# Kernel tuning notes

Hardware: AMD Instinct MI355X
Metric: run time of the kernel (lower is better)

Reference implementation:

```python
import jax, jax.numpy as jnp
import numpy as np

B, U = 2048, 4096
BUDGET_POS = 24.0
BUDGET_NEG = 24.0


def setup_inputs() -> dict:
    key = jax.random.key(0)
    k1, k2, k3 = jax.random.split(key, 3)
    unit_duration_exec = jax.random.uniform(k1, (B, U), dtype=jnp.float32) * 10.0
    source_duration_obs = jax.random.randint(k2, (B, U), 0, 20, dtype=jnp.int32)
    unit_mask = jnp.ones((B, U), dtype=jnp.float32)
    speech_commit_mask = jax.random.randint(k3, (B, U), 0, 2, dtype=jnp.int32)
    residual_prev = jnp.zeros((B, 1), dtype=jnp.float32)
    prefix_offset_prev = jnp.zeros((B, 1), dtype=jnp.float32)
    return {
        'unit_duration_exec': unit_duration_exec,
        'source_duration_obs': source_duration_obs,
        'unit_mask': unit_mask,
        'speech_commit_mask': speech_commit_mask,
        'residual_prev': residual_prev,
        'prefix_offset_prev': prefix_offset_prev,
    }


def _project_row(dur, src, cm, scm, carry0, off0):
    # Sequential per-unit duration clamp/carry scan for a single batch row.
    def step(carry, xs):
        c, off = carry
        d, s, m, sm = xs
        src_count = jnp.maximum(0.0, jnp.round(s))          # int(max(0, round(src)))
        total = jnp.maximum(0.0, d + c)
        frames0 = jnp.maximum(1.0, jnp.floor(total))
        anchor = jnp.maximum(1.0, src_count)
        lower = jnp.maximum(1.0, jnp.ceil(anchor - (BUDGET_NEG + off)))
        upper = jnp.maximum(lower, jnp.floor(anchor + (BUDGET_POS - off)))
        frames = jnp.clip(frames0, lower, upper)
        is_commit = m > 0.5
        is_speech = sm > 0.5
        active = is_commit & is_speech                        # committed speech unit
        proj = jnp.where(is_commit, jnp.where(is_speech, frames, src_count), 0.0)
        c_next = jnp.where(active, total - frames, c)
        off_next = jnp.where(active, off + frames - anchor, off)
        return (c_next, off_next), proj

    (c_f, off_f), proj = jax.lax.scan(step, (carry0, off0), (dur, src, cm, sm_f := scm))
    return proj, c_f, off_f


def reference(unit_duration_exec, source_duration_obs, unit_mask, speech_commit_mask,
              residual_prev, prefix_offset_prev):
    commit_mask = unit_mask  # sealed_mask is None -> commit_mask = unit_mask.float()
    src = source_duration_obs.astype(jnp.float32)
    scm = speech_commit_mask.astype(jnp.float32)
    carry0 = residual_prev[:, 0]
    off0 = jnp.round(prefix_offset_prev[:, 0])  # int(round(prev offset))

    projected, residual_next, offset_next = jax.vmap(_project_row)(
        unit_duration_exec, src, commit_mask, scm, carry0, off0)

    # materialized = x + stop_grad(projected*mask - x)  (straight-through)
    projected_prefix = projected * commit_mask
    materialized = unit_duration_exec + jax.lax.stop_gradient(
        projected_prefix - unit_duration_exec)
    cached_duration_exec = projected * commit_mask
    return (materialized, projected, cached_duration_exec,
            residual_next[:, None], offset_next[:, None])
```

## Files before the change

### kernel.cpp

```cpp
#include <hip/hip_runtime.h>
#include <stdint.h>


__device__ __forceinline__ float rl_f(float v, int lane) {
  return __int_as_float(__builtin_amdgcn_readlane(__float_as_int(v), lane));
}

__global__ __launch_bounds__(64, 2)
void sdp_scan_kernel(const float* __restrict__ dur, const int* __restrict__ src,
                     const float* __restrict__ um, const int* __restrict__ scm,
                     const float* __restrict__ res_prev,
                     const float* __restrict__ off_prev,
                     float* __restrict__ out, int B, int U) {
  const int row  = blockIdx.x;
  const int lane = threadIdx.x;

  const int tot = B * U;
  float* __restrict__ outM = out;
  float* __restrict__ outP = out + tot;
  float* __restrict__ outC = out + 2 * tot;

  float c = res_prev[row];
  float w = rintf(off_prev[row]) + 24.0f;

  const int rowbase = row * U;
  const int rowlast = rowbase + U - 1;
  const int ntiles  = (U + 63) >> 6;

  int u    = lane;
  int idx  = rowbase + lane;
  int idxc = idx <= rowlast ? idx : rowlast;
  float d = dur[idxc]; int s = src[idxc]; float m = um[idxc]; int q = scm[idxc];

  for (int tile = 0; tile < ntiles; ++tile) {
    const int nidx  = idx + 64;
    const int nidxc = nidx <= rowlast ? nidx : rowlast;
    float dn = dur[nidxc]; int sn = src[nidxc];
    float mn = um[nidxc];  int qn = scm[nidxc];
    __builtin_amdgcn_sched_barrier(0);

    const bool valid = u < U;
    const float srcc   = fmaxf(0.0f, (float)s);
    const float anchor = fmaxf(1.0f, srcc);
    const bool  ic     = m > 0.5f;
    const bool  act    = valid && ic && (q > 0);

    const unsigned long long bal = __ballot(act);
    const int n = __popcll(bal);
    const int below = __builtin_amdgcn_mbcnt_hi((unsigned)(bal >> 32),
                      __builtin_amdgcn_mbcnt_lo((unsigned)bal, 0));
    const int pidx = (act ? below : n + (lane - below)) << 2;
    const float vdc = __int_as_float(__builtin_amdgcn_ds_permute(pidx, __float_as_int(d)));
    const float vac = __int_as_float(__builtin_amdgcn_ds_permute(pidx, __float_as_int(anchor)));

    const float vprev = __int_as_float(
        __builtin_amdgcn_ds_bpermute(((lane - 1) & 63) << 2, __float_as_int(vac)));
    const unsigned long long condm = __ballot(vdc <= vprev);

    float projc = vac;
    int j = 0;
    while (j < n) {
      const float dj = rl_f(vdc, j);
      if (w == 0.0f && c + dj <= 0.0f) {
        const unsigned long long above =
            (j >= 63) ? 0ull : ((~condm) >> (j + 1));
        int mEnd = above ? (j + 1 + (int)__builtin_ctzll(above)) : 64;
        if (mEnd > n) mEnd = n;
        c = 0.0f - rl_f(vac, mEnd - 1);
        j = mEnd;
      } else {
        const float at = rl_f(vac, j);
        const float lo = at - w;
        const float up = lo + 48.0f;
        const float total  = fmaxf(0.0f, c + dj);
        const float f0     = fmaxf(1.0f, floorf(total));
        const float frames = fminf(fmaxf(f0, lo), up);
        c = total - frames;
        w = frames - lo;
        projc = (lane == j) ? frames : projc;
        ++j;
      }
    }

    const float pf = __int_as_float(
        __builtin_amdgcn_ds_bpermute(below << 2, __float_as_int(projc)));
    const float proj = act ? pf : (ic ? srcc : 0.0f);

    if (valid) {
      const float pm = proj * m;
      const float mt = d + (pm - d);
      outM[idx] = mt;
      outP[idx] = proj;
      outC[idx] = pm;
    }

    d = dn; s = sn; m = mn; q = qn;
    idx = nidx; u += 64;
  }

  if (lane == 0) {
    out[3 * tot + row]     = c;
    out[3 * tot + B + row] = w - 24.0f;
  }
}

extern "C" void kernel_launch(void* const* d_in, const int* in_sizes, int n_in,
                              void* d_out, int out_size, void* d_ws, size_t ws_size,
                              hipStream_t stream) {
  const float* dur      = (const float*)d_in[0];
  const int*   src      = (const int*)d_in[1];
  const float* um       = (const float*)d_in[2];
  const int*   scm      = (const int*)d_in[3];
  const float* res_prev = (const float*)d_in[4];
  const float* off_prev = (const float*)d_in[5];
  float* out = (float*)d_out;

  const int B = in_sizes[4];
  const int U = in_sizes[0] / B;

  dim3 grid(B);
  dim3 block(64);
  sdp_scan_kernel<<<grid, block, 0, stream>>>(dur, src, um, scm, res_prev, off_prev,
                                              out, B, U);
}
```

Measured before the change: 300.3 us.

## Split each row scan into speculative segments with a repair pass

Each row's sequential scan is split into 8 segments that run in parallel. Every segment starts from a guessed carry state taken from the last active unit of the previous tile, and it records its exit state after each tile. A second kernel walks the segments per row, checks whether the guessed entry state matches the true carry, and recomputes only the mismatched tiles until the state reconverges with the recorded one. This adds parallelism across the long serial row, at the cost of extra workspace traffic, a second launch, and possible rework when the speculation is wrong. The tile-level software prefetch of the old loop is dropped.

Result: faster. 249.3 us (-17.0%).

```diff
diff --git a/kernel.cpp b/kernel.cpp
--- a/kernel.cpp
+++ b/kernel.cpp
@@ -2,17 +2,89 @@
 #include <stdint.h>
 
 
+#define NSEG 8
+
 __device__ __forceinline__ float rl_f(float v, int lane) {
   return __int_as_float(__builtin_amdgcn_readlane(__float_as_int(v), lane));
 }
 
-__global__ __launch_bounds__(64, 2)
-void sdp_scan_kernel(const float* __restrict__ dur, const int* __restrict__ src,
+__device__ __forceinline__ void proc_tile(
+    const float* __restrict__ dur, const int* __restrict__ src,
+    const float* __restrict__ um, const int* __restrict__ scm,
+    float* __restrict__ outM, float* __restrict__ outP, float* __restrict__ outC,
+    int tilebase, int rowlast, int lane, float& c, float& w) {
+  const int  idx   = tilebase + lane;
+  const bool valid = idx <= rowlast;
+  const int  idxc  = valid ? idx : rowlast;
+  const float d = dur[idxc];
+  const int   s = src[idxc];
+  const float m = um[idxc];
+  const int   q = scm[idxc];
+
+  const float srcc   = fmaxf(0.0f, (float)s);
+  const float anchor = fmaxf(1.0f, srcc);
+  const bool  ic     = m > 0.5f;
+  const bool  act    = valid && ic && (q > 0);
+
+  const unsigned long long bal = __ballot(act);
+  const int n = __popcll(bal);
+  const int below = __builtin_amdgcn_mbcnt_hi((unsigned)(bal >> 32),
+                    __builtin_amdgcn_mbcnt_lo((unsigned)bal, 0));
+  const int pidx = (act ? below : n + (lane - below)) << 2;
+  const float vdc = __int_as_float(__builtin_amdgcn_ds_permute(pidx, __float_as_int(d)));
+  const float vac = __int_as_float(__builtin_amdgcn_ds_permute(pidx, __float_as_int(anchor)));
+  const float vprev = __int_as_float(
+      __builtin_amdgcn_ds_bpermute(((lane - 1) & 63) << 2, __float_as_int(vac)));
+  const unsigned long long condm = __ballot(vdc <= vprev);
+
+  float projc = vac;
+  int j = 0;
+  while (j < n) {
+    const float dj = rl_f(vdc, j);
+    if (w == 0.0f && c + dj <= 0.0f) {
+      const unsigned long long above = (j >= 63) ? 0ull : ((~condm) >> (j + 1));
+      int mEnd = above ? (j + 1 + (int)__builtin_ctzll(above)) : 64;
+      if (mEnd > n) mEnd = n;
+      c = 0.0f - rl_f(vac, mEnd - 1);
+      j = mEnd;
+    } else {
+      const float at = rl_f(vac, j);
+      const float lo = at - w;
+      const float up = lo + 48.0f;
+      const float total  = fmaxf(0.0f, c + dj);
+      const float f0     = fmaxf(1.0f, floorf(total));
+      const float frames = fminf(fmaxf(f0, lo), up);
+      c = total - frames;
+      w = frames - lo;
+      projc = (lane == j) ? frames : projc;
+      ++j;
+    }
+  }
+
+  const float pf = __int_as_float(
+      __builtin_amdgcn_ds_bpermute(below << 2, __float_as_int(projc)));
+  const float proj = act ? pf : (ic ? srcc : 0.0f);
+  if (valid) {
+    const float pm = __fmul_rn(proj, m);
+    const float mt = __fadd_rn(d, __fsub_rn(pm, d));
+    outM[idx] = mt;
+    outP[idx] = proj;
+    outC[idx] = pm;
+  }
+}
+
+__global__ __launch_bounds__(64, 8)
+void sdp_spec_kernel(const float* __restrict__ dur, const int* __restrict__ src,
                      const float* __restrict__ um, const int* __restrict__ scm,
                      const float* __restrict__ res_prev,
                      const float* __restrict__ off_prev,
-                     float* __restrict__ out, int B, int U) {
-  const int row  = blockIdx.x;
+                     float* __restrict__ out,
+                     float* __restrict__ wsExitC, float* __restrict__ wsExitW,
+                     float* __restrict__ wsGC, float* __restrict__ wsGW,
+                     int B, int U) {
+  const int bid  = blockIdx.x;
+  const int row  = bid >> 3;
+  const int seg  = bid & (NSEG - 1);
   const int lane = threadIdx.x;
 
   const int tot = B * U;
@@ -20,84 +92,127 @@
   float* __restrict__ outP = out + tot;
   float* __restrict__ outC = out + 2 * tot;
 
+  const int ntiles = (U + 63) >> 6;
+  const int tps    = (ntiles + NSEG - 1) / NSEG;
+  const int t0     = seg * tps;
+  if (t0 >= ntiles) return;
+  int t1 = t0 + tps; if (t1 > ntiles) t1 = ntiles;
+
+  const int rowbase = row * U;
+  const int rowlast = rowbase + U - 1;
+
+  float c, w;
+  if (seg == 0) {
+    c = res_prev[row];
+    w = rintf(off_prev[row]) + 24.0f;
+  } else {
+    const int gi = rowbase + t0 * 64 - 64 + lane;
+    const float mv = um[gi];
+    const int   qv = scm[gi];
+    const int   sv = src[gi];
+    const bool  a  = (mv > 0.5f) && (qv > 0);
+    const unsigned long long bal = __ballot(a);
+    if (bal) {
+      const int last = 63 - (int)__builtin_clzll(bal);
+      const float anch = fmaxf(1.0f, fmaxf(0.0f, (float)sv));
+      c = 0.0f - rl_f(anch, last);
+      w = 0.0f;
+    } else {
+      c = __int_as_float(0x7fc00000);
+      w = c;
+    }
+    if (lane == 0) { wsGC[row * NSEG + seg] = c; wsGW[row * NSEG + seg] = w; }
+  }
+
+  for (int t = t0; t < t1; ++t) {
+    proc_tile(dur, src, um, scm, outM, outP, outC, rowbase + t * 64, rowlast,
+              lane, c, w);
+    if (lane == 0) { wsExitC[row * ntiles + t] = c; wsExitW[row * ntiles + t] = w; }
+  }
+}
+
+__global__ __launch_bounds__(64, 2)
+void sdp_repair_kernel(const float* __restrict__ dur, const int* __restrict__ src,
+                       const float* __restrict__ um, const int* __restrict__ scm,
+                       const float* __restrict__ res_prev,
+                       const float* __restrict__ off_prev,
+                       float* __restrict__ out,
+                       const float* __restrict__ wsExitC,
+                       const float* __restrict__ wsExitW,
+                       const float* __restrict__ wsGC,
+                       const float* __restrict__ wsGW, int B, int U) {
+  const int row  = blockIdx.x;
+  const int lane = threadIdx.x;
+
+  const int tot = B * U;
+  float* __restrict__ outM = out;
+  float* __restrict__ outP = out + tot;
+  float* __restrict__ outC = out + 2 * tot;
+
+  const int ntiles  = (U + 63) >> 6;
+  const int tps     = (ntiles + NSEG - 1) / NSEG;
+  const int rowbase = row * U;
+  const int rowlast = rowbase + U - 1;
+
+  const float exC = (lane < ntiles) ? wsExitC[row * ntiles + lane] : 0.0f;
+  const float exW = (lane < ntiles) ? wsExitW[row * ntiles + lane] : 0.0f;
+  const float gC  = (lane < NSEG) ? wsGC[row * NSEG + lane] : 0.0f;
+  const float gW  = (lane < NSEG) ? wsGW[row * NSEG + lane] : 0.0f;
+
   float c = res_prev[row];
   float w = rintf(off_prev[row]) + 24.0f;
 
+  for (int seg = 0; seg < NSEG; ++seg) {
+    const int t0 = seg * tps;
+    if (t0 >= ntiles) break;
+    int t1 = t0 + tps; if (t1 > ntiles) t1 = ntiles;
+
+    bool match = (seg == 0);
+    if (!match) {
+      match = (__float_as_int(rl_f(gC, seg)) == __float_as_int(c)) &&
+              (__float_as_int(rl_f(gW, seg)) == __float_as_int(w));
+    }
+    if (match) {
+      c = rl_f(exC, t1 - 1); w = rl_f(exW, t1 - 1);
+    } else {
+      for (int t = t0; t < t1; ++t) {
+        proc_tile(dur, src, um, scm, outM, outP, outC, rowbase + t * 64, rowlast,
+                  lane, c, w);
+        if (__float_as_int(c) == __float_as_int(rl_f(exC, t)) &&
+            __float_as_int(w) == __float_as_int(rl_f(exW, t))) {
+          c = rl_f(exC, t1 - 1); w = rl_f(exW, t1 - 1);
+          break;
+        }
+      }
+    }
+  }
+
+  if (lane == 0) {
+    out[3 * tot + row]     = c;
+    out[3 * tot + B + row] = w - 24.0f;
+  }
+}
+
+__global__ __launch_bounds__(64, 2)
+void sdp_scan_fallback(const float* __restrict__ dur, const int* __restrict__ src,
+                       const float* __restrict__ um, const int* __restrict__ scm,
+                       const float* __restrict__ res_prev,
+                       const float* __restrict__ off_prev,
+                       float* __restrict__ out, int B, int U) {
+  const int row  = blockIdx.x;
+  const int lane = threadIdx.x;
+  const int tot  = B * U;
+  float* __restrict__ outM = out;
+  float* __restrict__ outP = out + tot;
+  float* __restrict__ outC = out + 2 * tot;
+  const int ntiles  = (U + 63) >> 6;
   const int rowbase = row * U;
   const int rowlast = rowbase + U - 1;
-  const int ntiles  = (U + 63) >> 6;
-
-  int u    = lane;
-  int idx  = rowbase + lane;
-  int idxc = idx <= rowlast ? idx : rowlast;
-  float d = dur[idxc]; int s = src[idxc]; float m = um[idxc]; int q = scm[idxc];
-
-  for (int tile = 0; tile < ntiles; ++tile) {
-    const int nidx  = idx + 64;
-    const int nidxc = nidx <= rowlast ? nidx : rowlast;
-    float dn = dur[nidxc]; int sn = src[nidxc];
-    float mn = um[nidxc];  int qn = scm[nidxc];
-    __builtin_amdgcn_sched_barrier(0);
-
-    const bool valid = u < U;
-    const float srcc   = fmaxf(0.0f, (float)s);
-    const float anchor = fmaxf(1.0f, srcc);
-    const bool  ic     = m > 0.5f;
-    const bool  act    = valid && ic && (q > 0);
-
-    const unsigned long long bal = __ballot(act);
-    const int n = __popcll(bal);
-    const int below = __builtin_amdgcn_mbcnt_hi((unsigned)(bal >> 32),
-                      __builtin_amdgcn_mbcnt_lo((unsigned)bal, 0));
-    const int pidx = (act ? below : n + (lane - below)) << 2;
-    const float vdc = __int_as_float(__builtin_amdgcn_ds_permute(pidx, __float_as_int(d)));
-    const float vac = __int_as_float(__builtin_amdgcn_ds_permute(pidx, __float_as_int(anchor)));
-
-    const float vprev = __int_as_float(
-        __builtin_amdgcn_ds_bpermute(((lane - 1) & 63) << 2, __float_as_int(vac)));
-    const unsigned long long condm = __ballot(vdc <= vprev);
-
-    float projc = vac;
-    int j = 0;
-    while (j < n) {
-      const float dj = rl_f(vdc, j);
-      if (w == 0.0f && c + dj <= 0.0f) {
-        const unsigned long long above =
-            (j >= 63) ? 0ull : ((~condm) >> (j + 1));
-        int mEnd = above ? (j + 1 + (int)__builtin_ctzll(above)) : 64;
-        if (mEnd > n) mEnd = n;
-        c = 0.0f - rl_f(vac, mEnd - 1);
-        j = mEnd;
-      } else {
-        const float at = rl_f(vac, j);
-        const float lo = at - w;
-        const float up = lo + 48.0f;
-        const float total  = fmaxf(0.0f, c + dj);
-        const float f0     = fmaxf(1.0f, floorf(total));
-        const float frames = fminf(fmaxf(f0, lo), up);
-        c = total - frames;
-        w = frames - lo;
-        projc = (lane == j) ? frames : projc;
-        ++j;
-      }
-    }
-
-    const float pf = __int_as_float(
-        __builtin_amdgcn_ds_bpermute(below << 2, __float_as_int(projc)));
-    const float proj = act ? pf : (ic ? srcc : 0.0f);
-
-    if (valid) {
-      const float pm = proj * m;
-      const float mt = d + (pm - d);
-      outM[idx] = mt;
-      outP[idx] = proj;
-      outC[idx] = pm;
-    }
-
-    d = dn; s = sn; m = mn; q = qn;
-    idx = nidx; u += 64;
-  }
-
+  float c = res_prev[row];
+  float w = rintf(off_prev[row]) + 24.0f;
+  for (int t = 0; t < ntiles; ++t)
+    proc_tile(dur, src, um, scm, outM, outP, outC, rowbase + t * 64, rowlast,
+              lane, c, w);
   if (lane == 0) {
     out[3 * tot + row]     = c;
     out[3 * tot + B + row] = w - 24.0f;
@@ -117,9 +232,22 @@
 
   const int B = in_sizes[4];
   const int U = in_sizes[0] / B;
-
-  dim3 grid(B);
-  dim3 block(64);
-  sdp_scan_kernel<<<grid, block, 0, stream>>>(dur, src, um, scm, res_prev, off_prev,
-                                              out, B, U);
-}
+  const int ntiles = (U + 63) >> 6;
+
+  const size_t need = (size_t)B * ntiles * 2 * sizeof(float) +
+                      (size_t)B * NSEG * 2 * sizeof(float);
+  if (ws_size >= need) {
+    float* wsExitC = (float*)d_ws;
+    float* wsExitW = wsExitC + (size_t)B * ntiles;
+    float* wsGC    = wsExitW + (size_t)B * ntiles;
+    float* wsGW    = wsGC + (size_t)B * NSEG;
+    sdp_spec_kernel<<<B * NSEG, 64, 0, stream>>>(dur, src, um, scm, res_prev,
+                                                 off_prev, out, wsExitC, wsExitW,
+                                                 wsGC, wsGW, B, U);
+    sdp_repair_kernel<<<B, 64, 0, stream>>>(dur, src, um, scm, res_prev, off_prev,
+                                            out, wsExitC, wsExitW, wsGC, wsGW, B, U);
+  } else {
+    sdp_scan_fallback<<<B, 64, 0, stream>>>(dur, src, um, scm, res_prev, off_prev,
+                                            out, B, U);
+  }
+}
```
